# Kernel tuning notes

Measured on AMD Instinct MI355X. Metric: run time of the kernel, lower is better.

## Reference

```python
import jax, jax.numpy as jnp
import numpy as np

N_RAYS = 65536
S = 192            # samples per ray (uniform segments for the reference)
N = N_RAYS * S
LAMBDA_OPACITY = 0.001
LAMBDA_DISTORTION = 0.001


def setup_inputs() -> dict:
    key = jax.random.key(0)
    ks = jax.random.split(key, 9)
    rgb_coarse = jax.random.uniform(ks[0], (N_RAYS, 3), dtype=jnp.float32)
    rgb_fine = jax.random.uniform(ks[1], (N_RAYS, 3), dtype=jnp.float32)
    rgb_target = jax.random.uniform(ks[2], (N_RAYS, 3), dtype=jnp.float32)
    depth = jax.random.uniform(ks[3], (N_RAYS,), dtype=jnp.float32)
    depth_target = jax.random.uniform(ks[4], (N_RAYS,), dtype=jnp.float32)
    opacity = jax.random.uniform(ks[5], (N_RAYS,), dtype=jnp.float32,
                                 minval=0.01, maxval=0.99)
    # sample weights roughly normalized per ray; positive intervals / midpoints
    ws = jax.random.uniform(ks[6], (N,), dtype=jnp.float32) / S
    deltas = jax.random.uniform(ks[7], (N,), dtype=jnp.float32) * 0.01
    ts = jax.random.uniform(ks[8], (N,), dtype=jnp.float32)
    ray_idx = jnp.arange(N_RAYS, dtype=jnp.int32)
    rays_a = jnp.stack([ray_idx, ray_idx * S,
                        jnp.full((N_RAYS,), S, dtype=jnp.int32)], axis=1)
    return {"rgb_coarse": rgb_coarse, "rgb_fine": rgb_fine,
            "rgb_target": rgb_target, "depth": depth,
            "depth_target": depth_target, "opacity": opacity,
            "ws": ws, "deltas": deltas, "ts": ts, "rays_a": rays_a}


def distortion_loss(ws, deltas, ts, rays_a):
    """Mip-NeRF 360 distortion loss per ray via inclusive/exclusive prefix scans.

    loss_r = sum_{i,j in r} w_i w_j |t_i - t_j| + (1/3) sum_{i in r} w_i^2 d_i
    computed as sum_i 2*w_i*(t_i*W_excl_i - (wt)_excl_i) + w_i^2 d_i / 3,
    where *_excl are within-ray exclusive prefix sums.
    """
    n_rays = rays_a.shape[0]
    starts = rays_a[:, 1]
    # segment id of each sample via its ray's start offset (starts are sorted)
    seg = jnp.searchsorted(starts, jnp.arange(ws.shape[0], dtype=starts.dtype),
                           side='right') - 1
    wts = ws * ts
    excl_w = jnp.cumsum(ws) - ws           # global exclusive prefix of w
    excl_wt = jnp.cumsum(wts) - wts        # global exclusive prefix of w*t
    # subtract prefix value at each segment's start -> within-ray exclusive scan
    w_prefix = excl_w - excl_w[starts][seg]
    wt_prefix = excl_wt - excl_wt[starts][seg]
    li = 2.0 * ws * (ts * w_prefix - wt_prefix) + ws * ws * deltas / 3.0
    loss_seg = jax.ops.segment_sum(li, seg, num_segments=n_rays)
    # place each segment's loss at its ray_idx
    return jnp.zeros(n_rays, ws.dtype).at[rays_a[:, 0]].add(loss_seg)


def reference(rgb_coarse, rgb_fine, rgb_target, depth, depth_target,
              opacity, ws, deltas, ts, rays_a):
    d_rgb = jnp.mean((rgb_coarse - rgb_target) ** 2, axis=1)
    d_rgb = d_rgb + jnp.mean((rgb_fine - rgb_target) ** 2, axis=1)
    d_depth = jnp.abs(depth - depth_target)
    o = opacity + 1e-10
    d_opacity = LAMBDA_OPACITY * (-o * jnp.log(o))
    d_distortion = LAMBDA_DISTORTION * distortion_loss(ws, deltas, ts, rays_a)
    return (d_rgb, d_depth, d_opacity, d_distortion)
```

## Files before the change

### kernel.cpp

```cpp
#include <hip/hip_runtime.h>
#include <math.h>

#define N_RAYS 65536
#define LAMBDA_OPACITY 0.001f
#define LAMBDA_DISTORTION 0.001f
#define RAYS_PER_BLOCK 4

__global__ __launch_bounds__(RAYS_PER_BLOCK * 64)
void distortion_kernel(
    const float* __restrict__ ws,
    const float* __restrict__ deltas,
    const float* __restrict__ ts,
    const int*   __restrict__ rays_a,
    float* __restrict__ out)
{
    const int wave = threadIdx.x >> 6;
    const int lane = threadIdx.x & 63;
    const int ray  = blockIdx.x * RAYS_PER_BLOCK + wave;
    if (ray >= N_RAYS) return;

    const int out_ray = rays_a[ray * 3 + 0];
    const int start   = rays_a[ray * 3 + 1];
    const int count   = rays_a[ray * 3 + 2];

    const int s0 = 3 * lane;
    const int p  = start + s0;
    const bool ok0 = (s0 + 0) < count;
    const bool ok1 = (s0 + 1) < count;
    const bool ok2 = (s0 + 2) < count;

    const float w0 = ok0 ? ws[p + 0] : 0.f;
    const float w1 = ok1 ? ws[p + 1] : 0.f;
    const float w2 = ok2 ? ws[p + 2] : 0.f;
    const float t0 = ok0 ? ts[p + 0] : 0.f;
    const float t1 = ok1 ? ts[p + 1] : 0.f;
    const float t2 = ok2 ? ts[p + 2] : 0.f;
    const float d0 = ok0 ? deltas[p + 0] : 0.f;
    const float d1 = ok1 ? deltas[p + 1] : 0.f;
    const float d2 = ok2 ? deltas[p + 2] : 0.f;

    const float wt0 = w0 * t0, wt1 = w1 * t1, wt2 = w2 * t2;

    const float lw  = w0 + w1 + w2;
    const float lwt = wt0 + wt1 + wt2;

    float iw = lw, iwt = lwt;
    #pragma unroll
    for (int off = 1; off < 64; off <<= 1) {
        float nw  = __shfl_up(iw,  off, 64);
        float nwt = __shfl_up(iwt, off, 64);
        if (lane >= off) { iw += nw; iwt += nwt; }
    }

    float e_w  = iw  - lw;
    float e_wt = iwt - lwt;

    float acc;
    acc  = 2.f * w0 * (t0 * e_w - e_wt) + w0 * w0 * d0 * (1.f / 3.f);
    e_w += w0; e_wt += wt0;
    acc += 2.f * w1 * (t1 * e_w - e_wt) + w1 * w1 * d1 * (1.f / 3.f);
    e_w += w1; e_wt += wt1;
    acc += 2.f * w2 * (t2 * e_w - e_wt) + w2 * w2 * d2 * (1.f / 3.f);

    #pragma unroll
    for (int off = 32; off > 0; off >>= 1)
        acc += __shfl_down(acc, off, 64);

    if (lane == 0)
        out[3 * N_RAYS + out_ray] = LAMBDA_DISTORTION * acc;
}

__global__ __launch_bounds__(256)
void perray_kernel(
    const float* __restrict__ rgb_coarse,
    const float* __restrict__ rgb_fine,
    const float* __restrict__ rgb_target,
    const float* __restrict__ depth,
    const float* __restrict__ depth_target,
    const float* __restrict__ opacity,
    float* __restrict__ out)
{
    const int r = blockIdx.x * blockDim.x + threadIdx.x;
    if (r >= N_RAYS) return;

    const float rt0 = rgb_target[r * 3 + 0];
    const float rt1 = rgb_target[r * 3 + 1];
    const float rt2 = rgb_target[r * 3 + 2];
    const float c0 = rgb_coarse[r * 3 + 0] - rt0;
    const float c1 = rgb_coarse[r * 3 + 1] - rt1;
    const float c2 = rgb_coarse[r * 3 + 2] - rt2;
    const float f0 = rgb_fine[r * 3 + 0] - rt0;
    const float f1 = rgb_fine[r * 3 + 1] - rt1;
    const float f2 = rgb_fine[r * 3 + 2] - rt2;

    out[r] = (c0 * c0 + c1 * c1 + c2 * c2) * (1.f / 3.f)
           + (f0 * f0 + f1 * f1 + f2 * f2) * (1.f / 3.f);

    out[N_RAYS + r] = fabsf(depth[r] - depth_target[r]);

    const float o = opacity[r] + 1e-10f;
    out[2 * N_RAYS + r] = LAMBDA_OPACITY * (-o * logf(o));
}

extern "C" void kernel_launch(void* const* d_in, const int* in_sizes, int n_in,
                              void* d_out, int out_size, void* d_ws, size_t ws_size,
                              hipStream_t stream) {
    const float* rgb_coarse   = (const float*)d_in[0];
    const float* rgb_fine     = (const float*)d_in[1];
    const float* rgb_target   = (const float*)d_in[2];
    const float* depth        = (const float*)d_in[3];
    const float* depth_target = (const float*)d_in[4];
    const float* opacity      = (const float*)d_in[5];
    const float* ws           = (const float*)d_in[6];
    const float* deltas       = (const float*)d_in[7];
    const float* ts           = (const float*)d_in[8];
    const int*   rays_a       = (const int*)d_in[9];
    float* out = (float*)d_out;

    const int grid_d = (N_RAYS + RAYS_PER_BLOCK - 1) / RAYS_PER_BLOCK;
    distortion_kernel<<<grid_d, RAYS_PER_BLOCK * 64, 0, stream>>>(
        ws, deltas, ts, rays_a, out);

    perray_kernel<<<N_RAYS / 256, 256, 0, stream>>>(
        rgb_coarse, rgb_fine, rgb_target, depth, depth_target, opacity, out);
}
```

Before: 180.0 us.

## Pack four rays per wavefront with 12 samples per lane and float4 loads

The distortion kernel now assigns 16 lanes per ray, so each wavefront handles four rays and each lane processes 12 contiguous samples. This shortens the shuffle scan and reduction from 6 to 4 steps and gives each lane more sequential work. When a lane's 12 samples are 16-byte aligned it loads them with float4 vector loads; otherwise it falls back to scalar loads. The cost is more registers per lane and a less coalesced access pattern, since each lane now strides 48 bytes apart.

```diff
diff --git a/kernel.cpp b/kernel.cpp
--- a/kernel.cpp
+++ b/kernel.cpp
@@ -4,9 +4,13 @@
 #define N_RAYS 65536
 #define LAMBDA_OPACITY 0.001f
 #define LAMBDA_DISTORTION 0.001f
-#define RAYS_PER_BLOCK 4
 
-__global__ __launch_bounds__(RAYS_PER_BLOCK * 64)
+#define WAVES_PER_BLOCK 4
+#define RAYS_PER_WAVE 4
+#define LANES_PER_RAY 16
+#define SAMPLES_PER_LANE 12
+
+__global__ __launch_bounds__(WAVES_PER_BLOCK * 64)
 void distortion_kernel(
     const float* __restrict__ ws,
     const float* __restrict__ deltas,
@@ -16,57 +20,73 @@
 {
     const int wave = threadIdx.x >> 6;
     const int lane = threadIdx.x & 63;
-    const int ray  = blockIdx.x * RAYS_PER_BLOCK + wave;
+    const int W    = blockIdx.x * WAVES_PER_BLOCK + wave;
+    const int g    = lane >> 4;
+    const int sl   = lane & 15;
+    const int ray  = W * RAYS_PER_WAVE + g;
     if (ray >= N_RAYS) return;
 
     const int out_ray = rays_a[ray * 3 + 0];
     const int start   = rays_a[ray * 3 + 1];
     const int count   = rays_a[ray * 3 + 2];
 
-    const int s0 = 3 * lane;
-    const int p  = start + s0;
-    const bool ok0 = (s0 + 0) < count;
-    const bool ok1 = (s0 + 1) < count;
-    const bool ok2 = (s0 + 2) < count;
+    const int s0 = sl * SAMPLES_PER_LANE;
 
-    const float w0 = ok0 ? ws[p + 0] : 0.f;
-    const float w1 = ok1 ? ws[p + 1] : 0.f;
-    const float w2 = ok2 ? ws[p + 2] : 0.f;
-    const float t0 = ok0 ? ts[p + 0] : 0.f;
-    const float t1 = ok1 ? ts[p + 1] : 0.f;
-    const float t2 = ok2 ? ts[p + 2] : 0.f;
-    const float d0 = ok0 ? deltas[p + 0] : 0.f;
-    const float d1 = ok1 ? deltas[p + 1] : 0.f;
-    const float d2 = ok2 ? deltas[p + 2] : 0.f;
+    float w[SAMPLES_PER_LANE], t[SAMPLES_PER_LANE], d[SAMPLES_PER_LANE];
 
-    const float wt0 = w0 * t0, wt1 = w1 * t1, wt2 = w2 * t2;
+    if (s0 + SAMPLES_PER_LANE <= count && (((start + s0) & 3) == 0)) {
+        const float4* wp = (const float4*)(ws     + start + s0);
+        const float4* tp = (const float4*)(ts     + start + s0);
+        const float4* dp = (const float4*)(deltas + start + s0);
+        #pragma unroll
+        for (int q = 0; q < 3; ++q) {
+            float4 vw = wp[q], vt = tp[q], vd = dp[q];
+            w[4*q+0] = vw.x; w[4*q+1] = vw.y; w[4*q+2] = vw.z; w[4*q+3] = vw.w;
+            t[4*q+0] = vt.x; t[4*q+1] = vt.y; t[4*q+2] = vt.z; t[4*q+3] = vt.w;
+            d[4*q+0] = vd.x; d[4*q+1] = vd.y; d[4*q+2] = vd.z; d[4*q+3] = vd.w;
+        }
+    } else {
+        #pragma unroll
+        for (int k = 0; k < SAMPLES_PER_LANE; ++k) {
+            const bool ok = (s0 + k) < count;
+            const int  p  = start + s0 + k;
+            w[k] = ok ? ws[p]     : 0.f;
+            t[k] = ok ? ts[p]     : 0.f;
+            d[k] = ok ? deltas[p] : 0.f;
+        }
+    }
 
-    const float lw  = w0 + w1 + w2;
-    const float lwt = wt0 + wt1 + wt2;
+    float lw = 0.f, lwt = 0.f;
+    #pragma unroll
+    for (int k = 0; k < SAMPLES_PER_LANE; ++k) {
+        lw  += w[k];
+        lwt += w[k] * t[k];
+    }
 
     float iw = lw, iwt = lwt;
     #pragma unroll
-    for (int off = 1; off < 64; off <<= 1) {
-        float nw  = __shfl_up(iw,  off, 64);
-        float nwt = __shfl_up(iwt, off, 64);
-        if (lane >= off) { iw += nw; iwt += nwt; }
+    for (int off = 1; off < LANES_PER_RAY; off <<= 1) {
+        float nw  = __shfl_up(iw,  off, LANES_PER_RAY);
+        float nwt = __shfl_up(iwt, off, LANES_PER_RAY);
+        if (sl >= off) { iw += nw; iwt += nwt; }
     }
 
     float e_w  = iw  - lw;
     float e_wt = iwt - lwt;
 
-    float acc;
-    acc  = 2.f * w0 * (t0 * e_w - e_wt) + w0 * w0 * d0 * (1.f / 3.f);
-    e_w += w0; e_wt += wt0;
-    acc += 2.f * w1 * (t1 * e_w - e_wt) + w1 * w1 * d1 * (1.f / 3.f);
-    e_w += w1; e_wt += wt1;
-    acc += 2.f * w2 * (t2 * e_w - e_wt) + w2 * w2 * d2 * (1.f / 3.f);
+    float acc = 0.f;
+    #pragma unroll
+    for (int k = 0; k < SAMPLES_PER_LANE; ++k) {
+        acc += 2.f * w[k] * (t[k] * e_w - e_wt) + w[k] * w[k] * d[k] * (1.f / 3.f);
+        e_w  += w[k];
+        e_wt += w[k] * t[k];
+    }
 
     #pragma unroll
-    for (int off = 32; off > 0; off >>= 1)
-        acc += __shfl_down(acc, off, 64);
+    for (int off = LANES_PER_RAY / 2; off > 0; off >>= 1)
+        acc += __shfl_down(acc, off, LANES_PER_RAY);
 
-    if (lane == 0)
+    if (sl == 0)
         out[3 * N_RAYS + out_ray] = LAMBDA_DISTORTION * acc;
 }
 
@@ -117,8 +137,9 @@
     const int*   rays_a       = (const int*)d_in[9];
     float* out = (float*)d_out;
 
-    const int grid_d = (N_RAYS + RAYS_PER_BLOCK - 1) / RAYS_PER_BLOCK;
-    distortion_kernel<<<grid_d, RAYS_PER_BLOCK * 64, 0, stream>>>(
+    const int rays_per_block = WAVES_PER_BLOCK * RAYS_PER_WAVE;
+    const int grid_d = (N_RAYS + rays_per_block - 1) / rays_per_block;
+    distortion_kernel<<<grid_d, WAVES_PER_BLOCK * 64, 0, stream>>>(
         ws, deltas, ts, rays_a, out);
 
     perray_kernel<<<N_RAYS / 256, 256, 0, stream>>>(
```

Result: no change. 181.3 us (+0.8%).

## Vectorize per-ray sample loads as float4 and use DPP wave scans

Applied to the files above, without the earlier changes.

Each lane now handles 4 contiguous samples instead of 3. When a ray has exactly 192 aligned samples, 48 lanes fetch ws, ts and deltas with float4 loads; otherwise a guarded scalar path runs. The shuffle-based prefix scan and reduction are replaced by DPP row-shift and row-broadcast adds, which avoid the LDS-permute path and the per-step branches. The aim is wider, better-coalesced memory transactions and cheaper intra-wave communication. The cost is that 16 lanes sit idle in the fast path, and the fallback only covers rays of up to 256 samples.

```diff
diff --git a/kernel.cpp b/kernel.cpp
--- a/kernel.cpp
+++ b/kernel.cpp
@@ -4,9 +4,25 @@
 #define N_RAYS 65536
 #define LAMBDA_OPACITY 0.001f
 #define LAMBDA_DISTORTION 0.001f
-#define RAYS_PER_BLOCK 4
 
-__global__ __launch_bounds__(RAYS_PER_BLOCK * 64)
+template <int CTRL, int ROW_MASK>
+__device__ __forceinline__ float dpp_add(float x) {
+    int s = __builtin_amdgcn_update_dpp(0, __float_as_int(x),
+                                        CTRL, ROW_MASK, 0xf, false);
+    return x + __int_as_float(s);
+}
+
+__device__ __forceinline__ float wave64_incl_scan(float x) {
+    x = dpp_add<0x111, 0xf>(x);
+    x = dpp_add<0x112, 0xf>(x);
+    x = dpp_add<0x114, 0xf>(x);
+    x = dpp_add<0x118, 0xf>(x);
+    x = dpp_add<0x142, 0xa>(x);
+    x = dpp_add<0x143, 0xc>(x);
+    return x;
+}
+
+__global__ __launch_bounds__(256)
 void distortion_kernel(
     const float* __restrict__ ws,
     const float* __restrict__ deltas,
@@ -14,60 +30,61 @@
     const int*   __restrict__ rays_a,
     float* __restrict__ out)
 {
-    const int wave = threadIdx.x >> 6;
     const int lane = threadIdx.x & 63;
-    const int ray  = blockIdx.x * RAYS_PER_BLOCK + wave;
+    const int ray  = blockIdx.x * 4 + (threadIdx.x >> 6);
     if (ray >= N_RAYS) return;
 
     const int out_ray = rays_a[ray * 3 + 0];
     const int start   = rays_a[ray * 3 + 1];
     const int count   = rays_a[ray * 3 + 2];
 
-    const int s0 = 3 * lane;
-    const int p  = start + s0;
-    const bool ok0 = (s0 + 0) < count;
-    const bool ok1 = (s0 + 1) < count;
-    const bool ok2 = (s0 + 2) < count;
+    float w[4] = {0.f, 0.f, 0.f, 0.f};
+    float t[4] = {0.f, 0.f, 0.f, 0.f};
+    float d[4] = {0.f, 0.f, 0.f, 0.f};
 
-    const float w0 = ok0 ? ws[p + 0] : 0.f;
-    const float w1 = ok1 ? ws[p + 1] : 0.f;
-    const float w2 = ok2 ? ws[p + 2] : 0.f;
-    const float t0 = ok0 ? ts[p + 0] : 0.f;
-    const float t1 = ok1 ? ts[p + 1] : 0.f;
-    const float t2 = ok2 ? ts[p + 2] : 0.f;
-    const float d0 = ok0 ? deltas[p + 0] : 0.f;
-    const float d1 = ok1 ? deltas[p + 1] : 0.f;
-    const float d2 = ok2 ? deltas[p + 2] : 0.f;
+    if (count == 192 && ((start & 3) == 0)) {
+        if (lane < 48) {
+            const float4 vw = *(const float4*)(ws     + start + 4 * lane);
+            const float4 vt = *(const float4*)(ts     + start + 4 * lane);
+            const float4 vd = *(const float4*)(deltas + start + 4 * lane);
+            __builtin_amdgcn_sched_barrier(0);
+            w[0] = vw.x; w[1] = vw.y; w[2] = vw.z; w[3] = vw.w;
+            t[0] = vt.x; t[1] = vt.y; t[2] = vt.z; t[3] = vt.w;
+            d[0] = vd.x; d[1] = vd.y; d[2] = vd.z; d[3] = vd.w;
+        }
+    } else {
+        #pragma unroll
+        for (int e = 0; e < 4; ++e) {
+            const int p  = 4 * lane + e;
+            const bool ok = p < count;
+            w[e] = ok ? ws[start + p]     : 0.f;
+            t[e] = ok ? ts[start + p]     : 0.f;
+            d[e] = ok ? deltas[start + p] : 0.f;
+        }
+    }
 
-    const float wt0 = w0 * t0, wt1 = w1 * t1, wt2 = w2 * t2;
+    const float wt0 = w[0] * t[0], wt1 = w[1] * t[1];
+    const float wt2 = w[2] * t[2], wt3 = w[3] * t[3];
+    const float lw  = (w[0] + w[1]) + (w[2] + w[3]);
+    const float lwt = (wt0 + wt1) + (wt2 + wt3);
 
-    const float lw  = w0 + w1 + w2;
-    const float lwt = wt0 + wt1 + wt2;
-
-    float iw = lw, iwt = lwt;
-    #pragma unroll
-    for (int off = 1; off < 64; off <<= 1) {
-        float nw  = __shfl_up(iw,  off, 64);
-        float nwt = __shfl_up(iwt, off, 64);
-        if (lane >= off) { iw += nw; iwt += nwt; }
-    }
+    const float iw  = wave64_incl_scan(lw);
+    const float iwt = wave64_incl_scan(lwt);
 
     float e_w  = iw  - lw;
     float e_wt = iwt - lwt;
 
-    float acc;
-    acc  = 2.f * w0 * (t0 * e_w - e_wt) + w0 * w0 * d0 * (1.f / 3.f);
-    e_w += w0; e_wt += wt0;
-    acc += 2.f * w1 * (t1 * e_w - e_wt) + w1 * w1 * d1 * (1.f / 3.f);
-    e_w += w1; e_wt += wt1;
-    acc += 2.f * w2 * (t2 * e_w - e_wt) + w2 * w2 * d2 * (1.f / 3.f);
+    float acc = 0.f;
+    #pragma unroll
+    for (int e = 0; e < 4; ++e) {
+        acc += 2.f * w[e] * (t[e] * e_w - e_wt) + w[e] * w[e] * d[e] * (1.f / 3.f);
+        e_w  += w[e];
+        e_wt += w[e] * t[e];
+    }
 
-    #pragma unroll
-    for (int off = 32; off > 0; off >>= 1)
-        acc += __shfl_down(acc, off, 64);
-
-    if (lane == 0)
-        out[3 * N_RAYS + out_ray] = LAMBDA_DISTORTION * acc;
+    const float tot = wave64_incl_scan(acc);
+    if (lane == 63)
+        out[3 * N_RAYS + out_ray] = LAMBDA_DISTORTION * tot;
 }
 
 __global__ __launch_bounds__(256)
@@ -117,8 +134,7 @@
     const int*   rays_a       = (const int*)d_in[9];
     float* out = (float*)d_out;
 
-    const int grid_d = (N_RAYS + RAYS_PER_BLOCK - 1) / RAYS_PER_BLOCK;
-    distortion_kernel<<<grid_d, RAYS_PER_BLOCK * 64, 0, stream>>>(
+    distortion_kernel<<<N_RAYS / 4, 256, 0, stream>>>(
         ws, deltas, ts, rays_a, out);
 
     perray_kernel<<<N_RAYS / 256, 256, 0, stream>>>(
```

New measurement: 179.5 us. Within noise of the previous version (-0.2%).
